# Optimization experiments

Measured on AMD Instinct MI355X. Metric: run time of the kernel, lower is better.

## Reference

```python
import jax, jax.numpy as jnp
import numpy as np

B, NR_BOX, D = 512, 18, 2048
NR_OBJ = NR_BOX - 2
K = 3
NUM_CLASSES = 174
NUM_CAT = 321


def setup_inputs() -> dict:
    key = jax.random.key(0)
    k1, k2, k3, k4, k5, k6 = jax.random.split(key, 6)
    obj_fea = jax.random.normal(k1, (B, NR_BOX, D), dtype=jnp.float32)
    # cooccurrence: nonnegative, sparse-ish, first (pad) column zero as in the torch code
    cooc = jax.random.uniform(k2, (NUM_CLASSES, NUM_CAT), dtype=jnp.float32)
    mask = jax.random.uniform(k3, (NUM_CLASSES, NUM_CAT)) < 0.5
    cooc = jnp.where(mask, cooc, 0.0).at[:, 0].set(0.0)
    obj_indicator = jax.random.randint(k4, (B, NR_BOX), 0, 2).astype(jnp.int32)
    obj_category = jax.random.randint(k5, (B, NR_BOX), 0, NUM_CAT).astype(jnp.int32)
    labels = jax.random.randint(k6, (B,), 0, NUM_CLASSES).astype(jnp.int32)
    return {
        'obj_fea': obj_fea,
        'cooccurrence': cooc,
        'obj_indicator': obj_indicator,
        'obj_category': obj_category,
        'labels': labels,
    }


def reference(obj_fea, cooccurrence, obj_indicator, obj_category, labels):
    Bn, nr_box, d = obj_fea.shape
    nr_obj = nr_box - 2
    ind = obj_indicator[:, 2:]          # (B, nr_obj)
    cats = obj_category[:, 2:]          # (B, nr_obj)
    ori_comp = obj_fea.mean(axis=1)     # (B, d)
    objs = obj_fea[:, 2:]               # (B, nr_obj, d), hands dropped
    label_onehot = jax.nn.one_hot(labels, NUM_CLASSES, dtype=obj_fea.dtype)  # (B, C)

    # W[i, b, j] = cooccurrence[labels[i], cats[b, j]]  (candidate weights per sample i)
    cooc_lab = cooccurrence[labels]                 # (B, NUM_CAT)
    W = cooc_lab[:, cats]                           # (B, B, nr_obj)
    eye = jnp.eye(Bn, dtype=bool)
    W = jnp.where(eye[:, :, None], 0.0, W)          # exclude own video (cand_obj[i] = 0)
    Wf = W.reshape(Bn, Bn * nr_obj)

    # softmax(log w) over nonzero support == w / sum(w); sample via categorical on log-weights
    logits = jnp.where(Wf > 0, jnp.log(jnp.where(Wf > 0, Wf, 1.0)), -jnp.inf)
    has_cand = (Wf > 0).any(axis=1) & (ind != 0).any(axis=1)  # (B,)

    rng = jax.random.key(42)
    r1, r2, r3 = jax.random.split(rng, 3)
    sel = jax.random.categorical(r1, logits, shape=(K, Bn)).T   # (B, K) flat candidate ids
    batch_idx = sel // nr_obj
    box_idx = sel % nr_obj
    sel_fea = objs[batch_idx, box_idx]              # (B, K, d)
    sel_label = label_onehot[batch_idx]             # (B, K, C)

    lam = jax.random.uniform(r2, (Bn, 1, 1), dtype=obj_fea.dtype)  # Beta(1,1)==U(0,1), one per sample
    slots = jax.random.randint(r3, (Bn, K), 0, nr_obj)
    own_fea = jnp.take_along_axis(objs, slots[:, :, None], axis=1)  # (B, K, d)

    mixed_fea = own_fea * lam + sel_fea * (1.0 - lam)
    mixed_label = label_onehot[:, None, :] * lam + sel_label * (1.0 - lam)

    # fallback path: mean of own objects + own one-hot label, repeated K times
    fb_fea = jnp.broadcast_to(objs.mean(axis=1)[:, None, :], mixed_fea.shape)
    fb_label = jnp.broadcast_to(label_onehot[:, None, :], mixed_label.shape)
    m = has_cand[:, None, None]
    mix_fea = jnp.where(m, mixed_fea, fb_fea)
    mix_label = jnp.where(m, mixed_label, fb_label)
    return ori_comp, mix_fea, mix_label
```

## Files before the change

kernel.cpp:

```cpp
#include <hip/hip_runtime.h>
#include <stdint.h>
#include <math.h>

#define NBOX 18
#define BB 512
#define DD 2048
#define NOBJ 16
#define KK 3
#define NCLS 174
#define NCAT 321
#define NCAND 8192
#define TINYF 1.1754943508222875e-38f

__host__ __device__ __forceinline__ uint32_t rotl32(uint32_t x, int d) {
  return (x << d) | (x >> (32 - d));
}

__host__ __device__ __forceinline__ void threefry2x32(uint32_t k0, uint32_t k1,
                                                      uint32_t x0, uint32_t x1,
                                                      uint32_t& o0, uint32_t& o1) {
  uint32_t ks2 = k0 ^ k1 ^ 0x1BD11BDAu;
  x0 += k0; x1 += k1;
#define TFR(r) x0 += x1; x1 = rotl32(x1, r); x1 ^= x0;
#define R4A TFR(13) TFR(15) TFR(26) TFR(6)
#define R4B TFR(17) TFR(29) TFR(16) TFR(24)
  R4A x0 += k1;  x1 += ks2 + 1u;
  R4B x0 += ks2; x1 += k0 + 2u;
  R4A x0 += k0;  x1 += k1 + 3u;
  R4B x0 += k1;  x1 += ks2 + 4u;
  R4A x0 += ks2; x1 += k0 + 5u;
#undef R4A
#undef R4B
#undef TFR
  o0 = x0; o1 = x1;
}

__device__ __forceinline__ float bits_to_unit(uint32_t bits) {
  float f = __uint_as_float((bits >> 9) | 0x3f800000u);
  return f - 1.0f;
}

__global__ __launch_bounds__(512) void prior_mix_kernel(
    const float* __restrict__ obj_fea, const float* __restrict__ cooc,
    const int* __restrict__ obj_ind, const int* __restrict__ obj_cat,
    const int* __restrict__ labels,
    uint32_t r1h, uint32_t r1l, uint32_t r2h, uint32_t r2l,
    uint32_t r3bh, uint32_t r3bl,
    float* __restrict__ ori, float* __restrict__ mixf, float* __restrict__ mixl) {
  const int b = blockIdx.x;
  const int tid = threadIdx.x;
  const int lane = tid & 63;
  const int wid = tid >> 6;

  __shared__ unsigned short jl[NCAND];
  __shared__ float wl[NCAND];
  __shared__ float pval[KK * 8];
  __shared__ int pidx[KK * 8];
  __shared__ int wtot[8];
  __shared__ int s_sel[KK];
  __shared__ int s_slots[KK];
  __shared__ float s_lam;
  __shared__ int s_hasc;

  const float4* fea4 = (const float4*)obj_fea;
  float4 v[NBOX];
#pragma unroll
  for (int r = 0; r < NBOX; ++r)
    v[r] = fea4[((size_t)b * NBOX + r) * 512 + tid];
  __builtin_amdgcn_sched_barrier(0);

  const int lab = labels[b];
  const float* crow = cooc + (size_t)lab * NCAT;
  const int seg = wid << 10;
  int cnt = 0;
#pragma unroll 1
  for (int c = 0; c < 16; ++c) {
    int j = seg + (c << 6) + lane;
    int jb = j >> 4;
    float w = 0.0f;
    if (jb != b) w = crow[obj_cat[jb * NBOX + 2 + (j & 15)]];
    unsigned long long m = __ballot(w > 0.0f);
    if (w > 0.0f) {
      int rank = __popcll(m & ((1ull << lane) - 1ull));
      int pos = seg + cnt + rank;
      jl[pos] = (unsigned short)j;
      wl[pos] = w;
    }
    cnt += __popcll(m);
  }
  if (lane == 0) wtot[wid] = cnt;

#pragma unroll 1
  for (int k = 0; k < KK; ++k) {
    uint32_t cbase = ((uint32_t)(k * BB + b)) << 13;
    float br = -1.0f;
    int bj = 0;
    for (int p = lane; p < cnt; p += 64) {
      uint32_t j = jl[seg + p];
      float w = wl[seg + p];
      uint32_t a0, a1;
      threefry2x32(r1h, r1l, 0u, cbase + j, a0, a1);
      float u = bits_to_unit(a0 ^ a1);
      if (u == 0.0f) u = TINYF;
      float t = -logf(u);
      if (w > br * t) { br = w / t; bj = (int)j; }
    }
#pragma unroll
    for (int mm = 1; mm < 64; mm <<= 1) {
      float ov = __shfl_xor(br, mm, 64);
      int oj = __shfl_xor(bj, mm, 64);
      if (ov > br || (ov == br && oj < bj)) { br = ov; bj = oj; }
    }
    if (lane == 0) { pval[k * 8 + wid] = br; pidx[k * 8 + wid] = bj; }
  }

  float4 S = v[0];
#pragma unroll
  for (int r = 1; r < NBOX; ++r) { S.x += v[r].x; S.y += v[r].y; S.z += v[r].z; S.w += v[r].w; }
  float4 S16;
  S16.x = S.x - v[0].x - v[1].x; S16.y = S.y - v[0].y - v[1].y;
  S16.z = S.z - v[0].z - v[1].z; S16.w = S.w - v[0].w - v[1].w;
  {
    const float is = 1.0f / 18.0f;
    float4 o; o.x = S.x * is; o.y = S.y * is; o.z = S.z * is; o.w = S.w * is;
    ((float4*)ori)[(size_t)b * 512 + tid] = o;
  }

  __syncthreads();

  if (tid == 0) {
    int total = 0;
#pragma unroll
    for (int w8 = 0; w8 < 8; ++w8) total += wtot[w8];
    int any = 0;
    for (int o = 0; o < NOBJ; ++o) any |= (obj_ind[b * NBOX + 2 + o] != 0);
    s_hasc = (total > 0) && any;
    for (int k = 0; k < KK; ++k) {
      float bv = -2.0f; int bj = 0;
      for (int w8 = 0; w8 < 8; ++w8) {
        float vv = pval[k * 8 + w8]; int jj = pidx[k * 8 + w8];
        if (vv > bv || (vv == bv && jj < bj)) { bv = vv; bj = jj; }
      }
      s_sel[k] = bj;
      uint32_t s0, s1;
      threefry2x32(r3bh, r3bl, 0u, (uint32_t)(b * KK + k), s0, s1);
      s_slots[k] = (int)((s0 ^ s1) & 15u);
    }
    uint32_t c0, c1;
    threefry2x32(r2h, r2l, 0u, (uint32_t)b, c0, c1);
    s_lam = bits_to_unit(c0 ^ c1);
  }
  __syncthreads();

  const int hc = s_hasc;
  const float l = s_lam, l1 = 1.0f - l;
  float4* mixf4 = (float4*)mixf;
  if (hc) {
#pragma unroll 1
    for (int k = 0; k < KK; ++k) {
      int s = s_sel[k];
      int bi = s >> 4, bo = s & 15, sl = s_slots[k];
      float4 a = fea4[((size_t)b * NBOX + 2 + sl) * 512 + tid];
      float4 e = fea4[((size_t)bi * NBOX + 2 + bo) * 512 + tid];
      float4 o;
      o.x = a.x * l + e.x * l1; o.y = a.y * l + e.y * l1;
      o.z = a.z * l + e.z * l1; o.w = a.w * l + e.w * l1;
      mixf4[((size_t)(b * KK + k)) * 512 + tid] = o;
    }
  } else {
    const float is = 1.0f / 16.0f;
    float4 o; o.x = S16.x * is; o.y = S16.y * is; o.z = S16.z * is; o.w = S16.w * is;
#pragma unroll
    for (int k = 0; k < KK; ++k) mixf4[((size_t)(b * KK + k)) * 512 + tid] = o;
  }
  if (tid < NCLS) {
    int lb = labels[b];
#pragma unroll 1
    for (int k = 0; k < KK; ++k) {
      float val;
      if (hc) {
        int ls = labels[s_sel[k] >> 4];
        val = (tid == lb ? l : 0.0f) + (tid == ls ? l1 : 0.0f);
      } else {
        val = (tid == lb) ? 1.0f : 0.0f;
      }
      mixl[(size_t)(b * KK + k) * NCLS + tid] = val;
    }
  }
}

extern "C" void kernel_launch(void* const* d_in, const int* in_sizes, int n_in,
                              void* d_out, int out_size, void* d_ws, size_t ws_size,
                              hipStream_t stream) {
  (void)in_sizes; (void)n_in; (void)out_size; (void)d_ws; (void)ws_size;
  const float* obj_fea = (const float*)d_in[0];
  const float* cooc    = (const float*)d_in[1];
  const int* obj_ind   = (const int*)d_in[2];
  const int* obj_cat   = (const int*)d_in[3];
  const int* labels    = (const int*)d_in[4];

  float* out  = (float*)d_out;
  float* ori  = out;
  float* mixf = out + (size_t)BB * DD;
  float* mixl = mixf + (size_t)BB * KK * DD;

  uint32_t r1h, r1l, r2h, r2l, r3h, r3l;
  threefry2x32(0u, 42u, 0u, 0u, r1h, r1l);
  threefry2x32(0u, 42u, 0u, 1u, r2h, r2l);
  threefry2x32(0u, 42u, 0u, 2u, r3h, r3l);
  uint32_t r3bh, r3bl;
  threefry2x32(r3h, r3l, 0u, 1u, r3bh, r3bl);

  hipLaunchKernelGGL(prior_mix_kernel, dim3(BB), dim3(512), 0, stream,
                     obj_fea, cooc, obj_ind, obj_cat, labels,
                     r1h, r1l, r2h, r2l, r3bh, r3bl,
                     ori, mixf, mixl);
}
```

Baseline: 47.35 us.

## Split sampling and feature mixing into two kernels with finer-grained parallel blocks

```diff
diff --git a/kernel.cpp b/kernel.cpp
--- a/kernel.cpp
+++ b/kernel.cpp
@@ -9,7 +9,8 @@
 #define KK 3
 #define NCLS 174
 #define NCAT 321
-#define NCAND 8192
+#define NQ 4
+#define QCAND 2048
 #define TINYF 1.1754943508222875e-38f
 
 __host__ __device__ __forceinline__ uint32_t rotl32(uint32_t x, int d) {
@@ -40,60 +41,49 @@
   return f - 1.0f;
 }
 
-__global__ __launch_bounds__(512) void prior_mix_kernel(
-    const float* __restrict__ obj_fea, const float* __restrict__ cooc,
-    const int* __restrict__ obj_ind, const int* __restrict__ obj_cat,
-    const int* __restrict__ labels,
-    uint32_t r1h, uint32_t r1l, uint32_t r2h, uint32_t r2l,
-    uint32_t r3bh, uint32_t r3bl,
-    float* __restrict__ ori, float* __restrict__ mixf, float* __restrict__ mixl) {
-  const int b = blockIdx.x;
+__global__ __launch_bounds__(256) void sample_kernel(
+    const float* __restrict__ cooc, const int* __restrict__ obj_cat,
+    const int* __restrict__ labels, uint32_t r1h, uint32_t r1l,
+    unsigned long long* __restrict__ part, int* __restrict__ cnts) {
+  const int gb = blockIdx.x;
+  const int b = gb >> 2;
+  const int q = gb & 3;
   const int tid = threadIdx.x;
   const int lane = tid & 63;
   const int wid = tid >> 6;
 
-  __shared__ unsigned short jl[NCAND];
-  __shared__ float wl[NCAND];
-  __shared__ float pval[KK * 8];
-  __shared__ int pidx[KK * 8];
-  __shared__ int wtot[8];
-  __shared__ int s_sel[KK];
-  __shared__ int s_slots[KK];
-  __shared__ float s_lam;
-  __shared__ int s_hasc;
-
-  const float4* fea4 = (const float4*)obj_fea;
-  float4 v[NBOX];
-#pragma unroll
-  for (int r = 0; r < NBOX; ++r)
-    v[r] = fea4[((size_t)b * NBOX + r) * 512 + tid];
-  __builtin_amdgcn_sched_barrier(0);
+  __shared__ unsigned short jl[QCAND];
+  __shared__ float wl[QCAND];
+  __shared__ float pv[KK * 4];
+  __shared__ int pj[KK * 4];
+  __shared__ int wc[4];
 
   const int lab = labels[b];
   const float* crow = cooc + (size_t)lab * NCAT;
-  const int seg = wid << 10;
+  const int seg = wid << 9;
+  const int jbase = (q << 11) + seg;
+
   int cnt = 0;
 #pragma unroll 1
-  for (int c = 0; c < 16; ++c) {
-    int j = seg + (c << 6) + lane;
+  for (int c = 0; c < 8; ++c) {
+    int j = jbase + (c << 6) + lane;
     int jb = j >> 4;
     float w = 0.0f;
     if (jb != b) w = crow[obj_cat[jb * NBOX + 2 + (j & 15)]];
     unsigned long long m = __ballot(w > 0.0f);
     if (w > 0.0f) {
       int rank = __popcll(m & ((1ull << lane) - 1ull));
-      int pos = seg + cnt + rank;
-      jl[pos] = (unsigned short)j;
-      wl[pos] = w;
+      jl[seg + cnt + rank] = (unsigned short)j;
+      wl[seg + cnt + rank] = w;
     }
     cnt += __popcll(m);
   }
-  if (lane == 0) wtot[wid] = cnt;
+  if (lane == 0) wc[wid] = cnt;
 
 #pragma unroll 1
   for (int k = 0; k < KK; ++k) {
     uint32_t cbase = ((uint32_t)(k * BB + b)) << 13;
-    float br = -1.0f;
+    float br = 0.0f;
     int bj = 0;
     for (int p = lane; p < cnt; p += 64) {
       uint32_t j = jl[seg + p];
@@ -111,48 +101,86 @@
       int oj = __shfl_xor(bj, mm, 64);
       if (ov > br || (ov == br && oj < bj)) { br = ov; bj = oj; }
     }
-    if (lane == 0) { pval[k * 8 + wid] = br; pidx[k * 8 + wid] = bj; }
-  }
-
-  float4 S = v[0];
-#pragma unroll
-  for (int r = 1; r < NBOX; ++r) { S.x += v[r].x; S.y += v[r].y; S.z += v[r].z; S.w += v[r].w; }
-  float4 S16;
-  S16.x = S.x - v[0].x - v[1].x; S16.y = S.y - v[0].y - v[1].y;
-  S16.z = S.z - v[0].z - v[1].z; S16.w = S.w - v[0].w - v[1].w;
+    if (lane == 0) { pv[k * 4 + wid] = br; pj[k * 4 + wid] = bj; }
+  }
+  __syncthreads();
+
+  if (tid == 0) {
+    cnts[gb] = wc[0] + wc[1] + wc[2] + wc[3];
+#pragma unroll
+    for (int k = 0; k < KK; ++k) {
+      float bv = pv[k * 4]; int bj = pj[k * 4];
+      for (int w4 = 1; w4 < 4; ++w4) {
+        float vv = pv[k * 4 + w4]; int jj = pj[k * 4 + w4];
+        if (vv > bv || (vv == bv && jj < bj)) { bv = vv; bj = jj; }
+      }
+      part[((size_t)b * KK + k) * NQ + q] =
+          ((unsigned long long)__float_as_uint(bv) << 32) | (uint32_t)(8192 - bj);
+    }
+  }
+}
+
+__global__ __launch_bounds__(256) void finish_kernel(
+    const float* __restrict__ obj_fea, const int* __restrict__ obj_ind,
+    const int* __restrict__ labels,
+    const unsigned long long* __restrict__ part, const int* __restrict__ cnts,
+    uint32_t r2h, uint32_t r2l, uint32_t r3bh, uint32_t r3bl,
+    float* __restrict__ ori, float* __restrict__ mixf, float* __restrict__ mixl) {
+  const int bx = blockIdx.x;
+  const int b = bx >> 1;
+  const int h = bx & 1;
+  const int tid = threadIdx.x;
+  const int off = (h << 8) + tid;
+
+  const float4* fea4 = (const float4*)obj_fea;
+  const size_t rbase = (size_t)b * NBOX * 512 + off;
+
+  float4 v0 = fea4[rbase];
+  float4 v1 = fea4[rbase + 512];
+  float4 S = make_float4(v0.x + v1.x, v0.y + v1.y, v0.z + v1.z, v0.w + v1.w);
+#pragma unroll
+  for (int r = 2; r < NBOX; ++r) {
+    float4 a = fea4[rbase + (size_t)r * 512];
+    S.x += a.x; S.y += a.y; S.z += a.z; S.w += a.w;
+  }
   {
     const float is = 1.0f / 18.0f;
-    float4 o; o.x = S.x * is; o.y = S.y * is; o.z = S.z * is; o.w = S.w * is;
-    ((float4*)ori)[(size_t)b * 512 + tid] = o;
-  }
-
-  __syncthreads();
-
-  if (tid == 0) {
-    int total = 0;
-#pragma unroll
-    for (int w8 = 0; w8 < 8; ++w8) total += wtot[w8];
+    float4 o = make_float4(S.x * is, S.y * is, S.z * is, S.w * is);
+    ((float4*)ori)[(size_t)b * 512 + off] = o;
+  }
+  float4 S16 = make_float4(S.x - v0.x - v1.x, S.y - v0.y - v1.y,
+                           S.z - v0.z - v1.z, S.w - v0.w - v1.w);
+
+  __shared__ int s_sel[KK];
+  __shared__ int s_slots[KK];
+  __shared__ float s_lam;
+  __shared__ int s_hc;
+  if (tid < KK) {
+    const int k = tid;
+    unsigned long long best = part[((size_t)b * KK + k) * NQ];
+#pragma unroll
+    for (int q = 1; q < NQ; ++q) {
+      unsigned long long p = part[((size_t)b * KK + k) * NQ + q];
+      if (p > best) best = p;
+    }
+    s_sel[k] = 8192 - (int)(best & 0xFFFFFFFFull);
+    uint32_t s0, s1;
+    threefry2x32(r3bh, r3bl, 0u, (uint32_t)(b * KK + k), s0, s1);
+    s_slots[k] = (int)((s0 ^ s1) & 15u);
+  } else if (tid == 3) {
+    int tot = cnts[b * NQ] + cnts[b * NQ + 1] + cnts[b * NQ + 2] + cnts[b * NQ + 3];
     int any = 0;
+#pragma unroll
     for (int o = 0; o < NOBJ; ++o) any |= (obj_ind[b * NBOX + 2 + o] != 0);
-    s_hasc = (total > 0) && any;
-    for (int k = 0; k < KK; ++k) {
-      float bv = -2.0f; int bj = 0;
-      for (int w8 = 0; w8 < 8; ++w8) {
-        float vv = pval[k * 8 + w8]; int jj = pidx[k * 8 + w8];
-        if (vv > bv || (vv == bv && jj < bj)) { bv = vv; bj = jj; }
-      }
-      s_sel[k] = bj;
-      uint32_t s0, s1;
-      threefry2x32(r3bh, r3bl, 0u, (uint32_t)(b * KK + k), s0, s1);
-      s_slots[k] = (int)((s0 ^ s1) & 15u);
-    }
+    s_hc = (tot > 0) && any;
+  } else if (tid == 4) {
     uint32_t c0, c1;
     threefry2x32(r2h, r2l, 0u, (uint32_t)b, c0, c1);
     s_lam = bits_to_unit(c0 ^ c1);
   }
   __syncthreads();
 
-  const int hc = s_hasc;
+  const int hc = s_hc;
   const float l = s_lam, l1 = 1.0f - l;
   float4* mixf4 = (float4*)mixf;
   if (hc) {
@@ -160,20 +188,21 @@
     for (int k = 0; k < KK; ++k) {
       int s = s_sel[k];
       int bi = s >> 4, bo = s & 15, sl = s_slots[k];
-      float4 a = fea4[((size_t)b * NBOX + 2 + sl) * 512 + tid];
-      float4 e = fea4[((size_t)bi * NBOX + 2 + bo) * 512 + tid];
+      float4 a = fea4[((size_t)b * NBOX + 2 + sl) * 512 + off];
+      float4 e = fea4[((size_t)bi * NBOX + 2 + bo) * 512 + off];
       float4 o;
       o.x = a.x * l + e.x * l1; o.y = a.y * l + e.y * l1;
       o.z = a.z * l + e.z * l1; o.w = a.w * l + e.w * l1;
-      mixf4[((size_t)(b * KK + k)) * 512 + tid] = o;
+      mixf4[((size_t)b * KK + k) * 512 + off] = o;
     }
   } else {
     const float is = 1.0f / 16.0f;
-    float4 o; o.x = S16.x * is; o.y = S16.y * is; o.z = S16.z * is; o.w = S16.w * is;
-#pragma unroll
-    for (int k = 0; k < KK; ++k) mixf4[((size_t)(b * KK + k)) * 512 + tid] = o;
-  }
-  if (tid < NCLS) {
+    float4 o = make_float4(S16.x * is, S16.y * is, S16.z * is, S16.w * is);
+#pragma unroll
+    for (int k = 0; k < KK; ++k) mixf4[((size_t)b * KK + k) * 512 + off] = o;
+  }
+
+  if (h == 0 && tid < NCLS) {
     int lb = labels[b];
 #pragma unroll 1
     for (int k = 0; k < KK; ++k) {
@@ -192,7 +221,7 @@
 extern "C" void kernel_launch(void* const* d_in, const int* in_sizes, int n_in,
                               void* d_out, int out_size, void* d_ws, size_t ws_size,
                               hipStream_t stream) {
-  (void)in_sizes; (void)n_in; (void)out_size; (void)d_ws; (void)ws_size;
+  (void)in_sizes; (void)n_in; (void)out_size; (void)ws_size;
   const float* obj_fea = (const float*)d_in[0];
   const float* cooc    = (const float*)d_in[1];
   const int* obj_ind   = (const int*)d_in[2];
@@ -203,6 +232,9 @@
   float* ori  = out;
   float* mixf = out + (size_t)BB * DD;
   float* mixl = mixf + (size_t)BB * KK * DD;
+
+  unsigned long long* part = (unsigned long long*)d_ws;
+  int* cnts = (int*)((char*)d_ws + (size_t)BB * KK * NQ * 8);
 
   uint32_t r1h, r1l, r2h, r2l, r3h, r3l;
   threefry2x32(0u, 42u, 0u, 0u, r1h, r1l);
@@ -211,8 +243,9 @@
   uint32_t r3bh, r3bl;
   threefry2x32(r3h, r3l, 0u, 1u, r3bh, r3bl);
 
-  hipLaunchKernelGGL(prior_mix_kernel, dim3(BB), dim3(512), 0, stream,
-                     obj_fea, cooc, obj_ind, obj_cat, labels,
-                     r1h, r1l, r2h, r2l, r3bh, r3bl,
-                     ori, mixf, mixl);
-}
+  hipLaunchKernelGGL(sample_kernel, dim3(BB * NQ), dim3(256), 0, stream,
+                     cooc, obj_cat, labels, r1h, r1l, part, cnts);
+  hipLaunchKernelGGL(finish_kernel, dim3(BB * 2), dim3(256), 0, stream,
+                     obj_fea, obj_ind, labels, part, cnts,
+                     r2h, r2l, r3bh, r3bl, ori, mixf, mixl);
+}
```

New measurement: 49.56 us. 4.7% more time.
